# Kernel tuning notes

Hardware: AMD Instinct MI355X
Metric: run time of the kernel (lower is better)

The kernel has to match this reference:

```python
import jax, jax.numpy as jnp
import numpy as np

B, T, N, F = 8, 32, 10000, 16
E = 160000
HG, HT = 64, 128
EPS = 1e-5


def setup_inputs() -> dict:
    key = jax.random.key(0)
    ks = jax.random.split(key, 12)
    s = lambda i, shape, sc=0.05: jax.random.normal(ks[i], shape, dtype=jnp.float32) * sc
    return {
        "x_seq": jax.random.normal(ks[0], (B, T, N, F), dtype=jnp.float32),
        "edge_index": jax.random.randint(ks[1], (2, E), 0, N),
        "W1l": s(2, (HG, F)), "b1": jnp.zeros((HG,), jnp.float32), "W1r": s(3, (HG, F)),
        "g1": jnp.ones((HG,), jnp.float32), "be1": jnp.zeros((HG,), jnp.float32),
        "W2l": s(4, (HG, HG)), "b2": jnp.zeros((HG,), jnp.float32), "W2r": s(5, (HG, HG)),
        "g2": jnp.ones((HG,), jnp.float32), "be2": jnp.zeros((HG,), jnp.float32),
        "W_ih": s(6, (3 * HT, HG)), "W_hh": s(7, (3 * HT, HT)),
        "b_ih": jnp.zeros((3 * HT,), jnp.float32), "b_hh": jnp.zeros((3 * HT,), jnp.float32),
        "Wh": s(8, (1, HT)), "bh": jnp.zeros((1,), jnp.float32),
    }


def _layernorm(h, g, b):
    mu = h.mean(-1, keepdims=True)
    var = ((h - mu) ** 2).mean(-1, keepdims=True)
    return (h - mu) * jax.lax.rsqrt(var + EPS) * g + b


def reference(x_seq, edge_index, W1l, b1, W1r, g1, be1, W2l, b2, W2r, g2, be2,
              W_ih, W_hh, b_ih, b_hh, Wh, bh):
    src, dst = edge_index[0], edge_index[1]
    deg = jax.ops.segment_sum(jnp.ones((E,), x_seq.dtype), dst, num_segments=N)
    inv_deg = (1.0 / jnp.maximum(deg, 1.0))[:, None]  # [N,1]

    def aggregate(x):  # x: [B,N,F] -> mean over incoming neighbors per node
        msgs = x[:, src, :]  # [B,E,F] gather
        agg = jax.vmap(lambda m: jax.ops.segment_sum(m, dst, num_segments=N))(msgs)
        return agg * inv_deg

    def sage(x, Wl, bl, Wr, g, b):
        # PyG SAGEConv(mean): lin_l(agg) + lin_r(x); then LayerNorm + ReLU (dropout=eval)
        h = aggregate(x) @ Wl.T + bl + x @ Wr.T
        return jax.nn.relu(_layernorm(h, g, b))

    def step(_, xt):  # xt: [B,N,F] -> pooled [B,HG]
        h = sage(xt, W1l, b1, W1r, g1, be1)
        h = sage(h, W2l, b2, W2r, g2, be2)
        return None, h.mean(axis=1)

    _, H = jax.lax.scan(step, None, jnp.swapaxes(x_seq, 0, 1))  # [T,B,HG]

    def gru_step(h, x):  # PyTorch GRU gate order: r, z, n
        gi = x @ W_ih.T + b_ih
        gh = h @ W_hh.T + b_hh
        ir, iz, in_ = jnp.split(gi, 3, axis=-1)
        hr, hz, hn = jnp.split(gh, 3, axis=-1)
        r = jax.nn.sigmoid(ir + hr)
        z = jax.nn.sigmoid(iz + hz)
        n = jnp.tanh(in_ + r * hn)
        return (1.0 - z) * n + z * h, None

    h0 = jnp.zeros((x_seq.shape[0], HT), x_seq.dtype)
    ht, _ = jax.lax.scan(gru_step, h0, H)
    return (ht @ Wh.T + bh).squeeze(-1)  # [B]
```

## Files before the change

### kernel.cpp

```cpp
#include <hip/hip_runtime.h>
#include <hip/hip_fp16.h>
#include <math.h>

#define B_ 8
#define T_ 32
#define N_ 10000
#define F_ 16
#define E_ 160000
#define HG_ 64
#define HT_ 128
#define BT_ (B_*T_)
#define PB_ 157
#define EPS_ 1e-5f
#define NR_ (N_+1)

typedef __attribute__((ext_vector_type(8))) _Float16 f16x8_t;
typedef __attribute__((ext_vector_type(4))) float f32x4_t;

__device__ inline unsigned short f2h(float f) {
  return __half_as_ushort(__float2half(f));
}
__device__ inline unsigned pkrtz_u(float a, float b) {
  auto h = __builtin_amdgcn_cvt_pkrtz(a, b);
  unsigned u; __builtin_memcpy(&u, &h, 4); return u;
}
__device__ inline unsigned pack2h(float a, float b) {
  __half2 h = __floats2half2_rn(a, b);
  unsigned u; __builtin_memcpy(&u, &h, 4); return u;
}
__device__ inline __half2 u2h(unsigned u) {
  __half2 h; __builtin_memcpy(&h, &u, 4); return h;
}
__device__ inline unsigned h2u(__half2 h) {
  unsigned u; __builtin_memcpy(&u, &h, 4); return u;
}
__device__ inline void bflyh(__half2& a, int m) {
  unsigned u = (unsigned)__shfl_xor((int)h2u(a), m);
  a += u2h(u);
}

__global__ void k_zero(int* p, int n) {
  int i = blockIdx.x * 256 + threadIdx.x;
  if (i < n) p[i] = 0;
}

__global__ void k_deg(const int* __restrict__ dst, int* __restrict__ deg) {
  int e = blockIdx.x * 256 + threadIdx.x;
  if (e < E_) atomicAdd(&deg[dst[e]], 1);
}

__global__ void k_scan(const int* __restrict__ deg, int* __restrict__ row_ptr,
                       float* __restrict__ inv_deg) {
  __shared__ int part[256];
  int tid = threadIdx.x;
  int base = tid * 40;
  int s = 0;
  for (int i = 0; i < 40; i++) { int idx = base + i; if (idx < N_) s += deg[idx]; }
  part[tid] = s;
  __syncthreads();
  if (tid == 0) {
    int run = 0;
    for (int i = 0; i < 256; i++) { int v = part[i]; part[i] = run; run += v; }
  }
  __syncthreads();
  int run = part[tid];
  for (int i = 0; i < 40; i++) {
    int idx = base + i;
    if (idx < N_) {
      row_ptr[idx] = run;
      int d = deg[idx];
      run += d;
      inv_deg[idx] = 1.0f / fmaxf((float)d, 1.0f);
    } else if (idx == N_) {
      row_ptr[N_] = run;
    }
  }
}

__global__ void k_fill(const int* __restrict__ src, const int* __restrict__ dst,
                       const int* __restrict__ row_ptr, int* __restrict__ cursor,
                       int* __restrict__ col) {
  int e = blockIdx.x * 256 + threadIdx.x;
  if (e < E_) {
    int d = dst[e];
    int p = atomicAdd(&cursor[d], 1);
    col[row_ptr[d] + p] = src[e];
  }
}

__global__ void k_prepw(const float* __restrict__ W2l, const float* __restrict__ W2r,
                        unsigned short* __restrict__ Wbf) {
  int idx = blockIdx.x * 256 + threadIdx.x;
  if (idx >= 4 * 4 * 64 * 8) return;
  int q  = idx & 7;
  int l  = (idx >> 3) & 63;
  int ks = (idx >> 9) & 3;
  int w  = idx >> 11;
  int j = w * 16 + (l & 15);
  int k = ks * 32 + ((l >> 4) * 8) + q;
  float v = (k < 64) ? W2l[j * 64 + k] : W2r[j * 64 + (k - 64)];
  Wbf[idx] = f2h(v);
}

__global__ void k_prepw1(const float* __restrict__ W1l, const float* __restrict__ W1r,
                         unsigned short* __restrict__ Wb1) {
  int idx = blockIdx.x * 256 + threadIdx.x;
  if (idx >= 4 * 64 * 8) return;
  int q = idx & 7;
  int l = (idx >> 3) & 63;
  int w = idx >> 9;
  int j = w * 16 + (l & 15);
  int k = ((l >> 4) * 8) + q;
  float v = (k < 16) ? W1l[j * 16 + k] : W1r[j * 16 + (k - 16)];
  Wb1[idx] = f2h(v);
}

__launch_bounds__(256, 8)
__global__ void k_sage1t(const float* __restrict__ x, const int* __restrict__ row_ptr,
                         const int* __restrict__ col, const float* __restrict__ inv_deg,
                         const unsigned short* __restrict__ Wb1, const float* __restrict__ b1,
                         const float* __restrict__ g1, const float* __restrict__ be1,
                         unsigned short* __restrict__ h1, const float* __restrict__ zrow,
                         int bt0, int CH, int swz) {
  __shared__ __align__(16) unsigned short ZU[64 * 136];
  __shared__ float red[2][4][64];
  unsigned short* Z1b = ZU;
  float* Zf = (float*)ZU;
  int i = blockIdx.x;
  int btl, chunk;
  if (swz) {
    int xcd = i & 7; int j = i >> 3; int per = CH >> 3;
    btl = xcd * per + j / PB_; chunk = j % PB_;
  } else {
    btl = i / PB_; chunk = i % PB_;
  }
  int bt = bt0 + btl;
  size_t xbase = (size_t)bt * (N_ * F_);
  int tid = threadIdx.x;
  int w = __builtin_amdgcn_readfirstlane(tid >> 6);
  int lane = tid & 63;
  int n0 = chunk * 64;
  int node = lane >> 4;
  int eo2 = (lane >> 2) & 3;
  int fq2 = lane & 3;
  const float4* x4b = (const float4*)(x + xbase);
  const float4* z4 = (const float4*)zrow;

  int nloc = n0 + w * 16 + (lane & 15);
  int rpA = 0, dS = 0; float ivS = 0.f;
  if (nloc < N_) { rpA = row_ptr[nloc]; dS = row_ptr[nloc + 1] - rpA; ivS = inv_deg[nloc]; }

  for (int p = 0; p < 4; ++p) {
    int mA = w * 16 + p * 4;
    int nA = n0 + mA;
    int s0My   = __shfl(rpA, p * 4 + node);
    int dMy    = __shfl(dS,  p * 4 + node);
    float ivMy = __shfl(ivS, p * 4 + node);
    int dcMy = dMy > 64 ? 64 : dMy;
    int tmx = max(dcMy, __shfl_xor(dcMy, 16));
    int mx  = max(tmx, __shfl_xor(tmx, 32));
    int rounds = (mx + 3) >> 2;
    int pos = lane & 15;
    int c0r = (pos      < dMy) ? col[s0My + pos]      : 0;
    int c1r = (pos + 16 < dMy) ? col[s0My + pos + 16] : 0;
    int c2r = (pos + 32 < dMy) ? col[s0My + pos + 32] : 0;
    int c3r = (pos + 48 < dMy) ? col[s0My + pos + 48] : 0;
    float4 a = {0.f, 0.f, 0.f, 0.f};
#define S1B(REG, BASE, RR)                                            \
    {                                                                 \
      int idx = eo2 + 4 * (RR);                                       \
      int s = __shfl(REG, (lane & 48) | (idx - (BASE)));              \
      const float4* bp = (idx < dcMy) ? (x4b + (size_t)s * 4) : z4;   \
      float4 v = bp[fq2];                                             \
      a.x += v.x; a.y += v.y; a.z += v.z; a.w += v.w;                 \
    }
    int rounds2 = (rounds + 1) & ~1;
    int r = 0;
    for (; r < rounds2 && r < 4;  r += 2) { S1B(c0r, 0, r)  S1B(c0r, 0, r + 1) }
    for (; r < rounds2 && r < 8;  r += 2) { S1B(c1r, 16, r) S1B(c1r, 16, r + 1) }
    for (; r < rounds2 && r < 12; r += 2) { S1B(c2r, 32, r) S1B(c2r, 32, r + 1) }
    for (; r < rounds2; r += 2)           { S1B(c3r, 48, r) S1B(c3r, 48, r + 1) }
#undef S1B
    if (dMy > 64) {
      for (int e = s0My + 64; e < s0My + dMy; ++e) {
        if (eo2 == 0) {
          float4 v = x4b[(size_t)col[e] * 4 + fq2];
          a.x += v.x; a.y += v.y; a.z += v.z; a.w += v.w;
        }
      }
    }
    a.x += __shfl_xor(a.x, 4);  a.y += __shfl_xor(a.y, 4);
    a.z += __shfl_xor(a.z, 4);  a.w += __shfl_xor(a.w, 4);
    a.x += __shfl_xor(a.x, 8);  a.y += __shfl_xor(a.y, 8);
    a.z += __shfl_xor(a.z, 8);  a.w += __shfl_xor(a.w, 8);
    if (eo2 == 0) {
      uint2 pk;
      pk.x = pkrtz_u(a.x * ivMy, a.y * ivMy);
      pk.y = pkrtz_u(a.z * ivMy, a.w * ivMy);
      *(uint2*)&Z1b[(mA + node) * 40 + fq2 * 4] = pk;
    } else if (eo2 == 1) {
      int nS = nA + node;
      float4 sv = {0.f, 0.f, 0.f, 0.f};
      if (nS < N_) sv = x4b[(size_t)nS * 4 + fq2];
      uint2 pk;
      pk.x = pkrtz_u(sv.x, sv.y);
      pk.y = pkrtz_u(sv.z, sv.w);
      *(uint2*)&Z1b[(mA + node) * 40 + 16 + fq2 * 4] = pk;
    }
  }
  __syncthreads();

  int g = lane >> 4, c = lane & 15;
  float bj = b1[w * 16 + c];
  f32x4_t accf[4];
#pragma unroll
  for (int mt = 0; mt < 4; ++mt) accf[mt] = (f32x4_t){bj, bj, bj, bj};
  f16x8_t bfr = ((const f16x8_t*)Wb1)[w * 64 + lane];
#pragma unroll
  for (int mt = 0; mt < 4; ++mt) {
    const f16x8_t* ap = (const f16x8_t*)&Z1b[(mt * 16 + c) * 40 + g * 8];
    accf[mt] = __builtin_amdgcn_mfma_f32_16x16x32_f16(*ap, bfr, accf[mt], 0, 0, 0);
  }
  __syncthreads();

#pragma unroll
  for (int mt = 0; mt < 4; ++mt) {
#pragma unroll
    for (int q = 0; q < 4; ++q) {
      int nodeq = mt * 16 + g * 4 + q;
      Zf[nodeq * 68 + w * 16 + c] = accf[mt][q];
    }
  }
  __syncthreads();

  int m = lane;
  const float* zr = Zf + m * 68 + w * 16;
  float4 z0 = *(const float4*)(zr + 0);
  float4 z1 = *(const float4*)(zr + 4);
  float4 z2 = *(const float4*)(zr + 8);
  float4 z3 = *(const float4*)(zr + 12);
  float acc[16];
  acc[0] = z0.x; acc[1] = z0.y; acc[2] = z0.z; acc[3] = z0.w;
  acc[4] = z1.x; acc[5] = z1.y; acc[6] = z1.z; acc[7] = z1.w;
  acc[8] = z2.x; acc[9] = z2.y; acc[10] = z2.z; acc[11] = z2.w;
  acc[12] = z3.x; acc[13] = z3.y; acc[14] = z3.z; acc[15] = z3.w;

  float s1 = 0.f, s2 = 0.f;
#pragma unroll
  for (int jj = 0; jj < 16; ++jj) { s1 += acc[jj]; s2 += acc[jj] * acc[jj]; }
  red[0][w][m] = s1;
  red[1][w][m] = s2;
  __syncthreads();
  float mu = (red[0][0][m] + red[0][1][m] + red[0][2][m] + red[0][3][m]) * (1.f / 64.f);
  float ex2 = (red[1][0][m] + red[1][1][m] + red[1][2][m] + red[1][3][m]) * (1.f / 64.f);
  float var = fmaxf(ex2 - mu * mu, 0.f);
  float rs = rsqrtf(var + EPS_);

  int nAbs = n0 + m;
  unsigned short* dst = h1 + ((size_t)btl * NR_ + nAbs) * HG_ + w * 16;
  if (nAbs < N_) {
#pragma unroll
    for (int jj = 0; jj < 16; ++jj)
      acc[jj] = fmaxf((acc[jj] - mu) * rs * g1[w * 16 + jj] + be1[w * 16 + jj], 0.f);
    uint4 pa, pb;
    pa.x = pack2h(acc[0], acc[1]);  pa.y = pack2h(acc[2], acc[3]);
    pa.z = pack2h(acc[4], acc[5]);  pa.w = pack2h(acc[6], acc[7]);
    pb.x = pack2h(acc[8], acc[9]);  pb.y = pack2h(acc[10], acc[11]);
    pb.z = pack2h(acc[12], acc[13]); pb.w = pack2h(acc[14], acc[15]);
    *(uint4*)dst = pa;
    *(uint4*)(dst + 8) = pb;
  } else if (nAbs == N_) {
    uint4 zz = {0, 0, 0, 0};
    *(uint4*)dst = zz;
    *(uint4*)(dst + 8) = zz;
  }
}

__launch_bounds__(256, 8)
__global__ void k_sage2t(const unsigned short* __restrict__ h1, const int* __restrict__ row_ptr,
                         const int* __restrict__ col, const float* __restrict__ inv_deg,
                         const unsigned short* __restrict__ Wbf, const float* __restrict__ b2,
                         const float* __restrict__ g2, const float* __restrict__ be2,
                         float* __restrict__ Hsum, int bt0, int CH, int swz) {
  __shared__ __align__(16) unsigned short Zb[64 * 136];
  __shared__ float red[2][4][64];
  float* Zf = (float*)Zb;
  int i = blockIdx.x;
  int btl, chunk;
  if (swz) {
    int xcd = i & 7; int j = i >> 3; int per = CH >> 3;
    btl = xcd * per + j / PB_; chunk = j % PB_;
  } else {
    btl = i / PB_; chunk = i % PB_;
  }
  int bt = bt0 + btl;
  int b = bt / T_, t = bt % T_;
  const char* h8c = (const char*)(h1 + (size_t)btl * (NR_ * HG_));
  int tid = threadIdx.x;
  int w = __builtin_amdgcn_readfirstlane(tid >> 6);
  int lane = tid & 63;
  int n0 = chunk * 64;
  int nsel = lane >> 5;
  int eo2 = (lane >> 3) & 3;
  int fq3 = lane & 7;
  unsigned foff = (unsigned)fq3 * 16;
  int pos = lane & 31;

  int nloc = n0 + w * 16 + (lane & 15);
  int rpA = 0, dS = 0; float ivS = 0.f;
  if (nloc < N_) { rpA = row_ptr[nloc]; dS = row_ptr[nloc + 1] - rpA; ivS = inv_deg[nloc]; }

  int cp0[8], cp1[8];
#pragma unroll
  for (int p = 0; p < 8; ++p) {
    int s0 = __shfl(rpA, p * 2 + nsel);
    int d  = __shfl(dS,  p * 2 + nsel);
    cp0[p] = (pos      < d) ? col[s0 + pos]      : N_;
    cp1[p] = (pos + 32 < d) ? col[s0 + pos + 32] : N_;
  }

#pragma unroll
  for (int p = 0; p < 8; ++p) {
    int mA = w * 16 + p * 2;
    int s0My   = __shfl(rpA, p * 2 + nsel);
    int dMy    = __shfl(dS,  p * 2 + nsel);
    float ivMy = __shfl(ivS, p * 2 + nsel);
    int dcMy = dMy > 64 ? 64 : dMy;
    int mx = max(dcMy, __shfl_xor(dcMy, 32));
    int rounds = (mx + 3) >> 2;
    __half2 a0 = __float2half2_rn(0.f), a1 = a0, a2 = a0, a3 = a0;
#define S2B(PREG, BASE, RR)                                             \
    {                                                                   \
      int idx = eo2 + 4 * (RR);                                         \
      int s = __shfl(PREG, (lane & 32) | (idx - (BASE)));               \
      uint4 v = *(const uint4*)(h8c + (((unsigned)s << 7) + foff));     \
      a0 += u2h(v.x); a1 += u2h(v.y); a2 += u2h(v.z); a3 += u2h(v.w);   \
    }
    int rounds2 = (rounds + 1) & ~1;
    int r = 0;
    for (; r < rounds2 && r < 8; r += 2) { S2B(cp0[p], 0, r)  S2B(cp0[p], 0, r + 1) }
    for (; r < rounds2; r += 2)          { S2B(cp1[p], 32, r) S2B(cp1[p], 32, r + 1) }
#undef S2B
    if (dMy > 64) {
      for (int e = s0My + 64; e < s0My + dMy; ++e) {
        if (eo2 == 0) {
          uint4 v = *(const uint4*)(h8c + (((unsigned)col[e] << 7) + foff));
          a0 += u2h(v.x); a1 += u2h(v.y); a2 += u2h(v.z); a3 += u2h(v.w);
        }
      }
    }
    bflyh(a0, 8);  bflyh(a1, 8);  bflyh(a2, 8);  bflyh(a3, 8);
    bflyh(a0, 16); bflyh(a1, 16); bflyh(a2, 16); bflyh(a3, 16);
    if (eo2 == 0) {
      __half2 ivh = __float2half2_rn(ivMy);
      uint4 pk;
      pk.x = h2u(a0 * ivh); pk.y = h2u(a1 * ivh);
      pk.z = h2u(a2 * ivh); pk.w = h2u(a3 * ivh);
      *(uint4*)&Zb[(mA + nsel) * 136 + fq3 * 8] = pk;
    } else if (eo2 == 1) {
      int nA = n0 + mA;
      int nS = nA + nsel;
      int nSc = nS < N_ ? nS : N_;
      uint4 sv = *(const uint4*)(h8c + (((unsigned)nSc << 7) + foff));
      *(uint4*)&Zb[(mA + nsel) * 136 + 64 + fq3 * 8] = sv;
    }
  }
  __syncthreads();

  int g = lane >> 4, c = lane & 15;
  const f16x8_t* Wb8 = (const f16x8_t*)Wbf;
  float bj = b2[w * 16 + c];
  f32x4_t accf[4];
#pragma unroll
  for (int mt = 0; mt < 4; ++mt) accf[mt] = (f32x4_t){bj, bj, bj, bj};
#pragma unroll
  for (int ks = 0; ks < 4; ++ks) {
    f16x8_t bfr = Wb8[(w * 4 + ks) * 64 + lane];
#pragma unroll
    for (int mt = 0; mt < 4; ++mt) {
      const f16x8_t* ap = (const f16x8_t*)&Zb[(mt * 16 + c) * 136 + ks * 32 + g * 8];
      accf[mt] = __builtin_amdgcn_mfma_f32_16x16x32_f16(*ap, bfr, accf[mt], 0, 0, 0);
    }
  }
  __syncthreads();

#pragma unroll
  for (int mt = 0; mt < 4; ++mt) {
#pragma unroll
    for (int q = 0; q < 4; ++q) {
      int nodeq = mt * 16 + g * 4 + q;
      Zf[nodeq * 68 + w * 16 + c] = accf[mt][q];
    }
  }
  __syncthreads();

  int m = lane;
  float* zr = Zf + m * 68 + w * 16;
  float4 z0 = *(const float4*)(zr + 0);
  float4 z1 = *(const float4*)(zr + 4);
  float4 z2 = *(const float4*)(zr + 8);
  float4 z3 = *(const float4*)(zr + 12);
  float acc[16];
  acc[0] = z0.x; acc[1] = z0.y; acc[2] = z0.z; acc[3] = z0.w;
  acc[4] = z1.x; acc[5] = z1.y; acc[6] = z1.z; acc[7] = z1.w;
  acc[8] = z2.x; acc[9] = z2.y; acc[10] = z2.z; acc[11] = z2.w;
  acc[12] = z3.x; acc[13] = z3.y; acc[14] = z3.z; acc[15] = z3.w;

  float s1 = 0.f, s2 = 0.f;
#pragma unroll
  for (int jj = 0; jj < 16; ++jj) { s1 += acc[jj]; s2 += acc[jj] * acc[jj]; }
  red[0][w][m] = s1;
  red[1][w][m] = s2;
  __syncthreads();
  float mu = (red[0][0][m] + red[0][1][m] + red[0][2][m] + red[0][3][m]) * (1.f / 64.f);
  float ex2 = (red[1][0][m] + red[1][1][m] + red[1][2][m] + red[1][3][m]) * (1.f / 64.f);
  float var = fmaxf(ex2 - mu * mu, 0.f);
  float rs = rsqrtf(var + EPS_);

  bool okm = (n0 + m) < N_;
#pragma unroll
  for (int jj = 0; jj < 16; ++jj) {
    float hv = fmaxf((acc[jj] - mu) * rs * g2[w * 16 + jj] + be2[w * 16 + jj], 0.f);
    acc[jj] = okm ? hv : 0.f;
  }
  float4 o0 = {acc[0], acc[1], acc[2], acc[3]};
  float4 o1 = {acc[4], acc[5], acc[6], acc[7]};
  float4 o2 = {acc[8], acc[9], acc[10], acc[11]};
  float4 o3 = {acc[12], acc[13], acc[14], acc[15]};
  *(float4*)(zr + 0) = o0;  *(float4*)(zr + 4) = o1;
  *(float4*)(zr + 8) = o2;  *(float4*)(zr + 12) = o3;
  __syncthreads();

  float cs = 0.f;
#pragma unroll
  for (int ii = 0; ii < 16; ++ii) cs += Zf[(w * 16 + ii) * 68 + lane];
  red[0][w][lane] = cs;
  __syncthreads();
  if (w == 0) {
    float tot = red[0][0][lane] + red[0][1][lane] + red[0][2][lane] + red[0][3][lane];
    atomicAdd(&Hsum[(t * B_ + b) * HG_ + lane], tot);
  }
}

__global__ void k_gi(const float* __restrict__ Hsum, const float* __restrict__ W_ih,
                     const float* __restrict__ b_ih, float* __restrict__ GI) {
  __shared__ float xv[64];
  int tb = blockIdx.x;
  int tid = threadIdx.x;
  if (tid < 64) xv[tid] = Hsum[tb * 64 + tid] * (1.0f / (float)N_);
  __syncthreads();
  float g = b_ih[tid];
  const float4* W4 = (const float4*)(W_ih + tid * 64);
  const float4* x4 = (const float4*)xv;
#pragma unroll
  for (int q = 0; q < 16; q++) {
    float4 w = W4[q], xq = x4[q];
    g = fmaf(xq.x, w.x, g); g = fmaf(xq.y, w.y, g);
    g = fmaf(xq.z, w.z, g); g = fmaf(xq.w, w.w, g);
  }
  GI[tb * 384 + tid] = g;
}

__global__ void k_gru(const float* __restrict__ GI, const float* __restrict__ W_hh,
                      const float* __restrict__ b_hh, const float* __restrict__ Wh,
                      const float* __restrict__ bh, float* __restrict__ out) {
  __shared__ float hL[128];
  __shared__ float ghL[384];
  __shared__ float red[128];
  int b = blockIdx.x, tid = threadIdx.x;
  if (tid < 128) hL[tid] = 0.f;
  float bhh = b_hh[tid];
  const float4* W4 = (const float4*)(W_hh + tid * 128);
  for (int t = 0; t < T_; ++t) {
    __syncthreads();
    float g = bhh;
    const float4* h4 = (const float4*)hL;
#pragma unroll
    for (int q = 0; q < 32; q++) {
      float4 w = W4[q], hv = h4[q];
      g = fmaf(hv.x, w.x, g); g = fmaf(hv.y, w.y, g);
      g = fmaf(hv.z, w.z, g); g = fmaf(hv.w, w.w, g);
    }
    ghL[tid] = g;
    __syncthreads();
    float hnew = 0.f;
    if (tid < 128) {
      const float* gi = GI + (t * B_ + b) * 384;
      float rr = 1.f / (1.f + expf(-(gi[tid] + ghL[tid])));
      float zz = 1.f / (1.f + expf(-(gi[128 + tid] + ghL[128 + tid])));
      float nn = tanhf(gi[256 + tid] + rr * ghL[256 + tid]);
      hnew = (1.f - zz) * nn + zz * hL[tid];
    }
    __syncthreads();
    if (tid < 128) hL[tid] = hnew;
  }
  __syncthreads();
  if (tid < 128) red[tid] = hL[tid] * Wh[tid];
  __syncthreads();
  if (tid == 0) {
    float s = bh[0];
    for (int k = 0; k < 128; k++) s += red[k];
    out[b] = s;
  }
}

extern "C" void kernel_launch(void* const* d_in, const int* in_sizes, int n_in,
                              void* d_out, int out_size, void* d_ws, size_t ws_size,
                              hipStream_t stream) {
  const float* x    = (const float*)d_in[0];
  const int*   ei   = (const int*)d_in[1];
  const float* W1l  = (const float*)d_in[2];
  const float* b1   = (const float*)d_in[3];
  const float* W1r  = (const float*)d_in[4];
  const float* g1   = (const float*)d_in[5];
  const float* be1  = (const float*)d_in[6];
  const float* W2l  = (const float*)d_in[7];
  const float* b2   = (const float*)d_in[8];
  const float* W2r  = (const float*)d_in[9];
  const float* g2   = (const float*)d_in[10];
  const float* be2  = (const float*)d_in[11];
  const float* W_ih = (const float*)d_in[12];
  const float* W_hh = (const float*)d_in[13];
  const float* b_ih = (const float*)d_in[14];
  const float* b_hh = (const float*)d_in[15];
  const float* Wh   = (const float*)d_in[16];
  const float* bh   = (const float*)d_in[17];
  float* out = (float*)d_out;

  char* ws = (char*)d_ws;
  size_t off = 0;
  auto alloc = [&](size_t bytes) { void* p = ws + off; off += (bytes + 255) & ~(size_t)255; return p; };
  int*   deg     = (int*)alloc((size_t)N_ * 4);
  int*   row_ptr = (int*)alloc((size_t)(N_ + 1) * 4);
  int*   cursor  = (int*)alloc((size_t)N_ * 4);
  int*   col     = (int*)alloc((size_t)E_ * 4);
  float* ivd     = (float*)alloc((size_t)N_ * 4);
  float* Hsum    = (float*)alloc((size_t)BT_ * HG_ * 4);
  float* GI      = (float*)alloc((size_t)BT_ * 384 * 4);
  unsigned short* Wbf = (unsigned short*)alloc((size_t)4 * 4 * 64 * 8 * 2);
  unsigned short* Wb1 = (unsigned short*)alloc((size_t)4 * 64 * 8 * 2);
  float* zrowp   = (float*)alloc(256);
  size_t fixed = off;
  unsigned short* h1 = (unsigned short*)(ws + off);

  size_t cap = (ws_size > fixed) ? (ws_size - fixed) : 0;
  int CH = (int)(cap / ((size_t)NR_ * HG_ * 2));
  if (CH > 64) CH = 64;
  if (CH >= 8) CH &= ~7;
  if (CH < 1) CH = 1;

  int zn = (int)(fixed / 4);
  k_zero<<<(zn + 255) / 256, 256, 0, stream>>>((int*)ws, zn);

  const int* srcp = ei;
  const int* dstp = ei + E_;
  k_deg<<<(E_ + 255) / 256, 256, 0, stream>>>(dstp, deg);
  k_scan<<<1, 256, 0, stream>>>(deg, row_ptr, ivd);
  k_fill<<<(E_ + 255) / 256, 256, 0, stream>>>(srcp, dstp, row_ptr, cursor, col);
  k_prepw<<<32, 256, 0, stream>>>(W2l, W2r, Wbf);
  k_prepw1<<<8, 256, 0, stream>>>(W1l, W1r, Wb1);

  for (int bt0 = 0; bt0 < BT_; bt0 += CH) {
    int c = BT_ - bt0 < CH ? BT_ - bt0 : CH;
    int swz = (c % 8 == 0) ? 1 : 0;
    k_sage1t<<<c * PB_, 256, 0, stream>>>(x, row_ptr, col, ivd, Wb1, b1, g1, be1,
                                          h1, zrowp, bt0, c, swz);
    k_sage2t<<<c * PB_, 256, 0, stream>>>(h1, row_ptr, col, ivd, Wbf, b2, g2, be2,
                                          Hsum, bt0, c, swz);
  }
  k_gi<<<BT_, 384, 0, stream>>>(Hsum, W_ih, b_ih, GI);
  k_gru<<<B_, 384, 0, stream>>>(GI, W_hh, b_hh, Wh, bh, out);
}
```

Before: 1.164 ms.

## Software-pipeline SAGE layers by fusing layer1 of chunk k with layer2 of chunk k-1

Merges the two SAGE layer kernels into one launch whose blocks pick a role: layer 1 for the current chunk of (batch,time) slices, or layer 2 for the previous chunk. The h1 intermediate is double-buffered, so the two stages work on different buffers and overlap inside one grid. Role assignment can be interleaved across XCD groups. This removes the serialization and tail idle between the separate layer launches and halves the launch count. The cost is a larger workspace, which caps the chunk size at 32 instead of 64, and register pressure from a kernel body holding both roles.

```diff
diff --git a/kernel.cpp b/kernel.cpp
--- a/kernel.cpp
+++ b/kernel.cpp
@@ -115,21 +115,19 @@
   Wb1[idx] = f2h(v);
 }
 
-__launch_bounds__(256, 8)
-__global__ void k_sage1t(const float* __restrict__ x, const int* __restrict__ row_ptr,
-                         const int* __restrict__ col, const float* __restrict__ inv_deg,
-                         const unsigned short* __restrict__ Wb1, const float* __restrict__ b1,
-                         const float* __restrict__ g1, const float* __restrict__ be1,
-                         unsigned short* __restrict__ h1, const float* __restrict__ zrow,
-                         int bt0, int CH, int swz) {
-  __shared__ __align__(16) unsigned short ZU[64 * 136];
-  __shared__ float red[2][4][64];
+__device__ __forceinline__ void sage1_body(
+    int i, unsigned short* ZU, float (*red)[4][64],
+    const float* __restrict__ x, const int* __restrict__ row_ptr,
+    const int* __restrict__ col, const float* __restrict__ inv_deg,
+    const unsigned short* __restrict__ Wb1, const float* __restrict__ b1,
+    const float* __restrict__ g1, const float* __restrict__ be1,
+    unsigned short* __restrict__ h1, const float* __restrict__ zrow,
+    int bt0, int CHc, int swz) {
   unsigned short* Z1b = ZU;
   float* Zf = (float*)ZU;
-  int i = blockIdx.x;
   int btl, chunk;
   if (swz) {
-    int xcd = i & 7; int j = i >> 3; int per = CH >> 3;
+    int xcd = i & 7; int j = i >> 3; int per = CHc >> 3;
     btl = xcd * per + j / PB_; chunk = j % PB_;
   } else {
     btl = i / PB_; chunk = i % PB_;
@@ -276,19 +274,18 @@
   }
 }
 
-__launch_bounds__(256, 8)
-__global__ void k_sage2t(const unsigned short* __restrict__ h1, const int* __restrict__ row_ptr,
-                         const int* __restrict__ col, const float* __restrict__ inv_deg,
-                         const unsigned short* __restrict__ Wbf, const float* __restrict__ b2,
-                         const float* __restrict__ g2, const float* __restrict__ be2,
-                         float* __restrict__ Hsum, int bt0, int CH, int swz) {
-  __shared__ __align__(16) unsigned short Zb[64 * 136];
-  __shared__ float red[2][4][64];
-  float* Zf = (float*)Zb;
-  int i = blockIdx.x;
+__device__ __forceinline__ void sage2_body(
+    int i, unsigned short* ZU, float (*red)[4][64],
+    const unsigned short* __restrict__ h1, const int* __restrict__ row_ptr,
+    const int* __restrict__ col, const float* __restrict__ inv_deg,
+    const unsigned short* __restrict__ Wbf, const float* __restrict__ b2,
+    const float* __restrict__ g2, const float* __restrict__ be2,
+    float* __restrict__ Hsum, int bt0, int CHc, int swz) {
+  unsigned short* Zb = ZU;
+  float* Zf = (float*)ZU;
   int btl, chunk;
   if (swz) {
-    int xcd = i & 7; int j = i >> 3; int per = CH >> 3;
+    int xcd = i & 7; int j = i >> 3; int per = CHc >> 3;
     btl = xcd * per + j / PB_; chunk = j % PB_;
   } else {
     btl = i / PB_; chunk = i % PB_;
@@ -440,6 +437,32 @@
     float tot = red[0][0][lane] + red[0][1][lane] + red[0][2][lane] + red[0][3][lane];
     atomicAdd(&Hsum[(t * B_ + b) * HG_ + lane], tot);
   }
+}
+
+__launch_bounds__(256, 8)
+__global__ void k_pipe(const float* __restrict__ x, const int* __restrict__ row_ptr,
+                       const int* __restrict__ col, const float* __restrict__ ivd,
+                       const unsigned short* __restrict__ Wb1, const float* __restrict__ b1,
+                       const float* __restrict__ g1, const float* __restrict__ be1,
+                       const unsigned short* __restrict__ Wbf, const float* __restrict__ b2,
+                       const float* __restrict__ g2, const float* __restrict__ be2,
+                       const unsigned short* __restrict__ h1in, unsigned short* __restrict__ h1out,
+                       float* __restrict__ Hsum, const float* __restrict__ zrow,
+                       int bt0_1, int c1, int swz1, int bt0_2, int c2, int swz2, int ilv) {
+  __shared__ __align__(16) unsigned short ZU[64 * 136];
+  __shared__ float red[2][4][64];
+  int i = blockIdx.x;
+  int role, li;
+  if (c1 == 0)      { role = 1; li = i; }
+  else if (c2 == 0) { role = 0; li = i; }
+  else if (ilv)     { int g = i >> 3; role = g & 1; li = ((g >> 1) << 3) | (i & 7); }
+  else              { int off = c1 * PB_; role = (i >= off) ? 1 : 0; li = role ? i - off : i; }
+  if (role == 0)
+    sage1_body(li, ZU, red, x, row_ptr, col, ivd, Wb1, b1, g1, be1, h1out, zrow,
+               bt0_1, c1, swz1);
+  else
+    sage2_body(li, ZU, red, h1in, row_ptr, col, ivd, Wbf, b2, g2, be2, Hsum,
+               bt0_2, c2, swz2);
 }
 
 __global__ void k_gi(const float* __restrict__ Hsum, const float* __restrict__ W_ih,
@@ -541,13 +564,16 @@
   unsigned short* Wb1 = (unsigned short*)alloc((size_t)4 * 64 * 8 * 2);
   float* zrowp   = (float*)alloc(256);
   size_t fixed = off;
-  unsigned short* h1 = (unsigned short*)(ws + off);
-
+
+  size_t rowb = (size_t)NR_ * HG_ * 2;
   size_t cap = (ws_size > fixed) ? (ws_size - fixed) : 0;
-  int CH = (int)(cap / ((size_t)NR_ * HG_ * 2));
-  if (CH > 64) CH = 64;
-  if (CH >= 8) CH &= ~7;
-  if (CH < 1) CH = 1;
+  int CHP = (int)(cap / (2 * rowb));
+  int CH;
+  if (CHP >= 32) CH = 32;
+  else if (CHP >= 8) CH = CHP & ~7;
+  else CH = CHP < 1 ? 1 : CHP;
+  unsigned short* h1a = (unsigned short*)(ws + fixed);
+  unsigned short* h1b = (unsigned short*)((char*)h1a + (size_t)CH * rowb);
 
   int zn = (int)(fixed / 4);
   k_zero<<<(zn + 255) / 256, 256, 0, stream>>>((int*)ws, zn);
@@ -560,13 +586,22 @@
   k_prepw<<<32, 256, 0, stream>>>(W2l, W2r, Wbf);
   k_prepw1<<<8, 256, 0, stream>>>(W1l, W1r, Wb1);
 
-  for (int bt0 = 0; bt0 < BT_; bt0 += CH) {
-    int c = BT_ - bt0 < CH ? BT_ - bt0 : CH;
-    int swz = (c % 8 == 0) ? 1 : 0;
-    k_sage1t<<<c * PB_, 256, 0, stream>>>(x, row_ptr, col, ivd, Wb1, b1, g1, be1,
-                                          h1, zrowp, bt0, c, swz);
-    k_sage2t<<<c * PB_, 256, 0, stream>>>(h1, row_ptr, col, ivd, Wbf, b2, g2, be2,
-                                          Hsum, bt0, c, swz);
+  int nch = (BT_ + CH - 1) / CH;
+  for (int k = 0; k <= nch; ++k) {
+    int b0_1 = k * CH;
+    int c1 = (k < nch) ? (BT_ - b0_1 < CH ? BT_ - b0_1 : CH) : 0;
+    int b0_2 = (k - 1) * CH;
+    int c2 = (k > 0) ? (BT_ - b0_2 < CH ? BT_ - b0_2 : CH) : 0;
+    unsigned short* h1out = (k & 1) ? h1b : h1a;
+    const unsigned short* h1in = (k & 1) ? h1a : h1b;
+    int swz1 = (c1 > 0 && (c1 % 8) == 0) ? 1 : 0;
+    int swz2 = (c2 > 0 && (c2 % 8) == 0) ? 1 : 0;
+    int ilv = (c1 == c2 && ((c1 * PB_) & 7) == 0) ? 1 : 0;
+    int grid = (c1 + c2) * PB_;
+    if (grid > 0)
+      k_pipe<<<grid, 256, 0, stream>>>(x, row_ptr, col, ivd, Wb1, b1, g1, be1,
+                                       Wbf, b2, g2, be2, h1in, h1out, Hsum, zrowp,
+                                       b0_1, c1, swz1, b0_2, c2, swz2, ilv);
   }
   k_gi<<<BT_, 384, 0, stream>>>(Hsum, W_ih, b_ih, GI);
   k_gru<<<B_, 384, 0, stream>>>(GI, W_hh, b_hh, Wh, bh, out);
```

Result: slower. 1.231 ms (+5.8%).

## Split aggregation from transforms and interleave 8 timesteps per node row

Applied to the files above, without the earlier changes.

Each SAGE layer is split into a gather-aggregation kernel and a dense MFMA transform kernel. Before gathering, inputs are repacked into a layout where each node row holds the features of 8 batch-time slots contiguously, so one neighbor index fetch serves 8 slices and each gather reads a wider contiguous row. This is meant to amortize CSR index loads and improve gather coalescing. In exchange it adds an extra transpose pass and intermediate buffers (xg, agg1, agg2) round-tripped through global memory, plus more kernel launches.

```diff
diff --git a/kernel.cpp b/kernel.cpp
--- a/kernel.cpp
+++ b/kernel.cpp
@@ -12,7 +12,8 @@
 #define BT_ (B_*T_)
 #define PB_ 157
 #define EPS_ 1e-5f
-#define NR_ (N_+1)
+#define NR2_ (PB_*64)
+#define NBTG_ 32
 
 typedef __attribute__((ext_vector_type(8))) _Float16 f16x8_t;
 typedef __attribute__((ext_vector_type(4))) float f32x4_t;
@@ -33,10 +34,6 @@
 }
 __device__ inline unsigned h2u(__half2 h) {
   unsigned u; __builtin_memcpy(&u, &h, 4); return u;
-}
-__device__ inline void bflyh(__half2& a, int m) {
-  unsigned u = (unsigned)__shfl_xor((int)h2u(a), m);
-  a += u2h(u);
 }
 
 __global__ void k_zero(int* p, int n) {
@@ -115,98 +112,138 @@
   Wb1[idx] = f2h(v);
 }
 
+__global__ void k_xg(const float* __restrict__ x, float* __restrict__ xg,
+                     int g0) {
+  int i = blockIdx.x;
+  int btgl = i / PB_, chunk = i % PB_;
+  int t = threadIdx.x;
+  int node = t >> 2, fq = t & 3;
+  int ng = chunk * 64 + node;
+  int nc = ng < N_ ? ng : N_ - 1;
+  float* ob = xg + ((size_t)btgl * NR2_ + ng) * 128 + fq * 4;
+#pragma unroll
+  for (int slot = 0; slot < 8; ++slot) {
+    int bt = (g0 + btgl) * 8 + slot;
+    float4 v = *(const float4*)(x + ((size_t)bt * N_ + nc) * 16 + fq * 4);
+    *(float4*)(ob + slot * 16) = v;
+  }
+}
+
 __launch_bounds__(256, 8)
-__global__ void k_sage1t(const float* __restrict__ x, const int* __restrict__ row_ptr,
-                         const int* __restrict__ col, const float* __restrict__ inv_deg,
-                         const unsigned short* __restrict__ Wb1, const float* __restrict__ b1,
-                         const float* __restrict__ g1, const float* __restrict__ be1,
-                         unsigned short* __restrict__ h1, const float* __restrict__ zrow,
-                         int bt0, int CH, int swz) {
+__global__ void k_agg1(const float* __restrict__ xg, const int* __restrict__ row_ptr,
+                       const int* __restrict__ col, const float* __restrict__ inv_deg,
+                       float* __restrict__ agg1) {
+  int i = blockIdx.x;
+  int btgl = i / PB_, chunk = i % PB_;
+  int tid = threadIdx.x;
+  int w = __builtin_amdgcn_readfirstlane(tid >> 6);
+  int lane = tid & 63;
+  int eo = lane >> 5, slot = (lane >> 2) & 7, fq = lane & 3;
+  const float* xb = xg + (size_t)btgl * NR2_ * 128;
+  float* ab = agg1 + (size_t)btgl * NR2_ * 128;
+  int nbase = chunk * 64 + w * 16;
+  unsigned off = (unsigned)slot * 16 + (unsigned)fq * 4;
+  for (int nn = 0; nn < 16; ++nn) {
+    int dn = nbase + nn;
+    float4 acc = {0.f, 0.f, 0.f, 0.f};
+    int dd = 0, s0 = 0; float iv = 0.f;
+    if (dn < N_) { s0 = row_ptr[dn]; dd = row_ptr[dn + 1] - s0; iv = inv_deg[dn]; }
+    for (int base = 0; base < dd; base += 64) {
+      int cnt = dd - base; if (cnt > 64) cnt = 64;
+      int cl = (lane < cnt) ? col[s0 + base + lane] : 0;
+      for (int e = 0; e < cnt; e += 2) {
+        int idx = e + eo;
+        int s = __shfl(cl, idx);
+        if (idx < cnt) {
+          float4 v = *(const float4*)(xb + (size_t)s * 128 + off);
+          acc.x += v.x; acc.y += v.y; acc.z += v.z; acc.w += v.w;
+        }
+      }
+    }
+    acc.x += __shfl_xor(acc.x, 32); acc.y += __shfl_xor(acc.y, 32);
+    acc.z += __shfl_xor(acc.z, 32); acc.w += __shfl_xor(acc.w, 32);
+    if (eo == 0) {
+      acc.x *= iv; acc.y *= iv; acc.z *= iv; acc.w *= iv;
+      *(float4*)(ab + (size_t)dn * 128 + off) = acc;
+    }
+  }
+}
+
+__launch_bounds__(256, 8)
+__global__ void k_agg2(const unsigned short* __restrict__ h1g, const int* __restrict__ row_ptr,
+                       const int* __restrict__ col, const float* __restrict__ inv_deg,
+                       unsigned short* __restrict__ agg2) {
+  int i = blockIdx.x;
+  int btgl = i / PB_, chunk = i % PB_;
+  int tid = threadIdx.x;
+  int w = __builtin_amdgcn_readfirstlane(tid >> 6);
+  int lane = tid & 63;
+  int slot = lane >> 3, fq3 = lane & 7;
+  const char* hb = (const char*)(h1g + (size_t)btgl * NR2_ * 512);
+  char* ab = (char*)(agg2 + (size_t)btgl * NR2_ * 512);
+  int nbase = chunk * 64 + w * 16;
+  unsigned off = (unsigned)slot * 128 + (unsigned)fq3 * 16;
+  for (int nn = 0; nn < 16; ++nn) {
+    int dn = nbase + nn;
+    __half2 a0 = __float2half2_rn(0.f), a1 = a0, a2 = a0, a3 = a0;
+    int dd = 0, s0 = 0; float iv = 0.f;
+    if (dn < N_) { s0 = row_ptr[dn]; dd = row_ptr[dn + 1] - s0; iv = inv_deg[dn]; }
+    for (int base = 0; base < dd; base += 64) {
+      int cnt = dd - base; if (cnt > 64) cnt = 64;
+      int cl = (lane < cnt) ? col[s0 + base + lane] : 0;
+      int e = 0;
+      for (; e + 1 < cnt; e += 2) {
+        int sA = __shfl(cl, e), sB = __shfl(cl, e + 1);
+        uint4 vA = *(const uint4*)(hb + (((size_t)sA) << 10) + off);
+        uint4 vB = *(const uint4*)(hb + (((size_t)sB) << 10) + off);
+        a0 += u2h(vA.x); a1 += u2h(vA.y); a2 += u2h(vA.z); a3 += u2h(vA.w);
+        a0 += u2h(vB.x); a1 += u2h(vB.y); a2 += u2h(vB.z); a3 += u2h(vB.w);
+      }
+      if (e < cnt) {
+        int sA = __shfl(cl, e);
+        uint4 vA = *(const uint4*)(hb + (((size_t)sA) << 10) + off);
+        a0 += u2h(vA.x); a1 += u2h(vA.y); a2 += u2h(vA.z); a3 += u2h(vA.w);
+      }
+    }
+    __half2 ivh = __float2half2_rn(iv);
+    uint4 pk;
+    pk.x = h2u(a0 * ivh); pk.y = h2u(a1 * ivh);
+    pk.z = h2u(a2 * ivh); pk.w = h2u(a3 * ivh);
+    *(uint4*)(ab + (((size_t)dn) << 10) + off) = pk;
+  }
+}
+
+__launch_bounds__(256, 8)
+__global__ void k_tr1(const float* __restrict__ x, const float* __restrict__ agg1,
+                      const unsigned short* __restrict__ Wb1, const float* __restrict__ b1,
+                      const float* __restrict__ g1, const float* __restrict__ be1,
+                      unsigned short* __restrict__ h1g, int g0) {
   __shared__ __align__(16) unsigned short ZU[64 * 136];
   __shared__ float red[2][4][64];
   unsigned short* Z1b = ZU;
   float* Zf = (float*)ZU;
   int i = blockIdx.x;
-  int btl, chunk;
-  if (swz) {
-    int xcd = i & 7; int j = i >> 3; int per = CH >> 3;
-    btl = xcd * per + j / PB_; chunk = j % PB_;
-  } else {
-    btl = i / PB_; chunk = i % PB_;
-  }
-  int bt = bt0 + btl;
-  size_t xbase = (size_t)bt * (N_ * F_);
+  int btl = i / PB_, chunk = i % PB_;
+  int bt = g0 * 8 + btl;
+  int btgl = btl >> 3, slot = btl & 7;
   int tid = threadIdx.x;
   int w = __builtin_amdgcn_readfirstlane(tid >> 6);
   int lane = tid & 63;
   int n0 = chunk * 64;
-  int node = lane >> 4;
-  int eo2 = (lane >> 2) & 3;
-  int fq2 = lane & 3;
-  const float4* x4b = (const float4*)(x + xbase);
-  const float4* z4 = (const float4*)zrow;
-
-  int nloc = n0 + w * 16 + (lane & 15);
-  int rpA = 0, dS = 0; float ivS = 0.f;
-  if (nloc < N_) { rpA = row_ptr[nloc]; dS = row_ptr[nloc + 1] - rpA; ivS = inv_deg[nloc]; }
-
-  for (int p = 0; p < 4; ++p) {
-    int mA = w * 16 + p * 4;
-    int nA = n0 + mA;
-    int s0My   = __shfl(rpA, p * 4 + node);
-    int dMy    = __shfl(dS,  p * 4 + node);
-    float ivMy = __shfl(ivS, p * 4 + node);
-    int dcMy = dMy > 64 ? 64 : dMy;
-    int tmx = max(dcMy, __shfl_xor(dcMy, 16));
-    int mx  = max(tmx, __shfl_xor(tmx, 32));
-    int rounds = (mx + 3) >> 2;
-    int pos = lane & 15;
-    int c0r = (pos      < dMy) ? col[s0My + pos]      : 0;
-    int c1r = (pos + 16 < dMy) ? col[s0My + pos + 16] : 0;
-    int c2r = (pos + 32 < dMy) ? col[s0My + pos + 32] : 0;
-    int c3r = (pos + 48 < dMy) ? col[s0My + pos + 48] : 0;
-    float4 a = {0.f, 0.f, 0.f, 0.f};
-#define S1B(REG, BASE, RR)                                            \
-    {                                                                 \
-      int idx = eo2 + 4 * (RR);                                       \
-      int s = __shfl(REG, (lane & 48) | (idx - (BASE)));              \
-      const float4* bp = (idx < dcMy) ? (x4b + (size_t)s * 4) : z4;   \
-      float4 v = bp[fq2];                                             \
-      a.x += v.x; a.y += v.y; a.z += v.z; a.w += v.w;                 \
-    }
-    int rounds2 = (rounds + 1) & ~1;
-    int r = 0;
-    for (; r < rounds2 && r < 4;  r += 2) { S1B(c0r, 0, r)  S1B(c0r, 0, r + 1) }
-    for (; r < rounds2 && r < 8;  r += 2) { S1B(c1r, 16, r) S1B(c1r, 16, r + 1) }
-    for (; r < rounds2 && r < 12; r += 2) { S1B(c2r, 32, r) S1B(c2r, 32, r + 1) }
-    for (; r < rounds2; r += 2)           { S1B(c3r, 48, r) S1B(c3r, 48, r + 1) }
-#undef S1B
-    if (dMy > 64) {
-      for (int e = s0My + 64; e < s0My + dMy; ++e) {
-        if (eo2 == 0) {
-          float4 v = x4b[(size_t)col[e] * 4 + fq2];
-          a.x += v.x; a.y += v.y; a.z += v.z; a.w += v.w;
-        }
-      }
-    }
-    a.x += __shfl_xor(a.x, 4);  a.y += __shfl_xor(a.y, 4);
-    a.z += __shfl_xor(a.z, 4);  a.w += __shfl_xor(a.w, 4);
-    a.x += __shfl_xor(a.x, 8);  a.y += __shfl_xor(a.y, 8);
-    a.z += __shfl_xor(a.z, 8);  a.w += __shfl_xor(a.w, 8);
-    if (eo2 == 0) {
-      uint2 pk;
-      pk.x = pkrtz_u(a.x * ivMy, a.y * ivMy);
-      pk.y = pkrtz_u(a.z * ivMy, a.w * ivMy);
-      *(uint2*)&Z1b[(mA + node) * 40 + fq2 * 4] = pk;
-    } else if (eo2 == 1) {
-      int nS = nA + node;
-      float4 sv = {0.f, 0.f, 0.f, 0.f};
-      if (nS < N_) sv = x4b[(size_t)nS * 4 + fq2];
-      uint2 pk;
-      pk.x = pkrtz_u(sv.x, sv.y);
-      pk.y = pkrtz_u(sv.z, sv.w);
-      *(uint2*)&Z1b[(mA + node) * 40 + 16 + fq2 * 4] = pk;
-    }
+
+  {
+    int m = w * 16 + (lane >> 2), fq2 = lane & 3;
+    int ng = n0 + m;
+    const float* ab = agg1 + (size_t)btgl * NR2_ * 128;
+    float4 av = *(const float4*)(ab + (size_t)ng * 128 + slot * 16 + fq2 * 4);
+    float4 sv = {0.f, 0.f, 0.f, 0.f};
+    if (ng < N_) sv = *(const float4*)(x + ((size_t)bt * N_ + ng) * 16 + fq2 * 4);
+    uint2 pka;
+    pka.x = pkrtz_u(av.x, av.y);  pka.y = pkrtz_u(av.z, av.w);
+    *(uint2*)&Z1b[m * 40 + fq2 * 4] = pka;
+    uint2 pks;
+    pks.x = pkrtz_u(sv.x, sv.y);  pks.y = pkrtz_u(sv.z, sv.w);
+    *(uint2*)&Z1b[m * 40 + 16 + fq2 * 4] = pks;
   }
   __syncthreads();
 
@@ -257,7 +294,7 @@
   float rs = rsqrtf(var + EPS_);
 
   int nAbs = n0 + m;
-  unsigned short* dst = h1 + ((size_t)btl * NR_ + nAbs) * HG_ + w * 16;
+  unsigned short* dst = h1g + ((size_t)btgl * NR2_ + nAbs) * 512 + slot * 64 + w * 16;
   if (nAbs < N_) {
 #pragma unroll
     for (int jj = 0; jj < 16; ++jj)
@@ -269,7 +306,7 @@
     pb.z = pack2h(acc[12], acc[13]); pb.w = pack2h(acc[14], acc[15]);
     *(uint4*)dst = pa;
     *(uint4*)(dst + 8) = pb;
-  } else if (nAbs == N_) {
+  } else {
     uint4 zz = {0, 0, 0, 0};
     *(uint4*)dst = zz;
     *(uint4*)(dst + 8) = zz;
@@ -277,92 +314,36 @@
 }
 
 __launch_bounds__(256, 8)
-__global__ void k_sage2t(const unsigned short* __restrict__ h1, const int* __restrict__ row_ptr,
-                         const int* __restrict__ col, const float* __restrict__ inv_deg,
-                         const unsigned short* __restrict__ Wbf, const float* __restrict__ b2,
-                         const float* __restrict__ g2, const float* __restrict__ be2,
-                         float* __restrict__ Hsum, int bt0, int CH, int swz) {
+__global__ void k_tr2(const unsigned short* __restrict__ h1g, const unsigned short* __restrict__ agg2,
+                      const unsigned short* __restrict__ Wbf, const float* __restrict__ b2,
+                      const float* __restrict__ g2, const float* __restrict__ be2,
+                      float* __restrict__ Hsum, int g0) {
   __shared__ __align__(16) unsigned short Zb[64 * 136];
   __shared__ float red[2][4][64];
   float* Zf = (float*)Zb;
   int i = blockIdx.x;
-  int btl, chunk;
-  if (swz) {
-    int xcd = i & 7; int j = i >> 3; int per = CH >> 3;
-    btl = xcd * per + j / PB_; chunk = j % PB_;
-  } else {
-    btl = i / PB_; chunk = i % PB_;
-  }
-  int bt = bt0 + btl;
+  int btl = i / PB_, chunk = i % PB_;
+  int bt = g0 * 8 + btl;
+  int btgl = btl >> 3, slot = btl & 7;
   int b = bt / T_, t = bt % T_;
-  const char* h8c = (const char*)(h1 + (size_t)btl * (NR_ * HG_));
   int tid = threadIdx.x;
   int w = __builtin_amdgcn_readfirstlane(tid >> 6);
   int lane = tid & 63;
   int n0 = chunk * 64;
-  int nsel = lane >> 5;
-  int eo2 = (lane >> 3) & 3;
-  int fq3 = lane & 7;
-  unsigned foff = (unsigned)fq3 * 16;
-  int pos = lane & 31;
-
-  int nloc = n0 + w * 16 + (lane & 15);
-  int rpA = 0, dS = 0; float ivS = 0.f;
-  if (nloc < N_) { rpA = row_ptr[nloc]; dS = row_ptr[nloc + 1] - rpA; ivS = inv_deg[nloc]; }
-
-  int cp0[8], cp1[8];
-#pragma unroll
-  for (int p = 0; p < 8; ++p) {
-    int s0 = __shfl(rpA, p * 2 + nsel);
-    int d  = __shfl(dS,  p * 2 + nsel);
-    cp0[p] = (pos      < d) ? col[s0 + pos]      : N_;
-    cp1[p] = (pos + 32 < d) ? col[s0 + pos + 32] : N_;
-  }
-
-#pragma unroll
-  for (int p = 0; p < 8; ++p) {
-    int mA = w * 16 + p * 2;
-    int s0My   = __shfl(rpA, p * 2 + nsel);
-    int dMy    = __shfl(dS,  p * 2 + nsel);
-    float ivMy = __shfl(ivS, p * 2 + nsel);
-    int dcMy = dMy > 64 ? 64 : dMy;
-    int mx = max(dcMy, __shfl_xor(dcMy, 32));
-    int rounds = (mx + 3) >> 2;
-    __half2 a0 = __float2half2_rn(0.f), a1 = a0, a2 = a0, a3 = a0;
-#define S2B(PREG, BASE, RR)                                             \
-    {                                                                   \
-      int idx = eo2 + 4 * (RR);                                         \
-      int s = __shfl(PREG, (lane & 32) | (idx - (BASE)));               \
-      uint4 v = *(const uint4*)(h8c + (((unsigned)s << 7) + foff));     \
-      a0 += u2h(v.x); a1 += u2h(v.y); a2 += u2h(v.z); a3 += u2h(v.w);   \
-    }
-    int rounds2 = (rounds + 1) & ~1;
-    int r = 0;
-    for (; r < rounds2 && r < 8; r += 2) { S2B(cp0[p], 0, r)  S2B(cp0[p], 0, r + 1) }
-    for (; r < rounds2; r += 2)          { S2B(cp1[p], 32, r) S2B(cp1[p], 32, r + 1) }
-#undef S2B
-    if (dMy > 64) {
-      for (int e = s0My + 64; e < s0My + dMy; ++e) {
-        if (eo2 == 0) {
-          uint4 v = *(const uint4*)(h8c + (((unsigned)col[e] << 7) + foff));
-          a0 += u2h(v.x); a1 += u2h(v.y); a2 += u2h(v.z); a3 += u2h(v.w);
-        }
-      }
-    }
-    bflyh(a0, 8);  bflyh(a1, 8);  bflyh(a2, 8);  bflyh(a3, 8);
-    bflyh(a0, 16); bflyh(a1, 16); bflyh(a2, 16); bflyh(a3, 16);
-    if (eo2 == 0) {
-      __half2 ivh = __float2half2_rn(ivMy);
-      uint4 pk;
-      pk.x = h2u(a0 * ivh); pk.y = h2u(a1 * ivh);
-      pk.z = h2u(a2 * ivh); pk.w = h2u(a3 * ivh);
-      *(uint4*)&Zb[(mA + nsel) * 136 + fq3 * 8] = pk;
-    } else if (eo2 == 1) {
-      int nA = n0 + mA;
-      int nS = nA + nsel;
-      int nSc = nS < N_ ? nS : N_;
-      uint4 sv = *(const uint4*)(h8c + (((unsigned)nSc << 7) + foff));
-      *(uint4*)&Zb[(mA + nsel) * 136 + 64 + fq3 * 8] = sv;
+
+  {
+    int mh = lane >> 3, fq3 = lane & 7;
+    const char* ab = (const char*)(agg2 + (size_t)btgl * NR2_ * 512);
+    const char* hb = (const char*)(h1g + (size_t)btgl * NR2_ * 512);
+    unsigned off = (unsigned)slot * 128 + (unsigned)fq3 * 16;
+#pragma unroll
+    for (int p = 0; p < 2; ++p) {
+      int m = w * 16 + p * 8 + mh;
+      size_t ro = (((size_t)(n0 + m)) << 10) + off;
+      uint4 va = *(const uint4*)(ab + ro);
+      uint4 vs = *(const uint4*)(hb + ro);
+      *(uint4*)&Zb[m * 136 + fq3 * 8] = va;
+      *(uint4*)&Zb[m * 136 + 64 + fq3 * 8] = vs;
     }
   }
   __syncthreads();
@@ -539,15 +520,21 @@
   float* GI      = (float*)alloc((size_t)BT_ * 384 * 4);
   unsigned short* Wbf = (unsigned short*)alloc((size_t)4 * 4 * 64 * 8 * 2);
   unsigned short* Wb1 = (unsigned short*)alloc((size_t)4 * 64 * 8 * 2);
-  float* zrowp   = (float*)alloc(256);
   size_t fixed = off;
-  unsigned short* h1 = (unsigned short*)(ws + off);
-
+
+  size_t xg_b = (size_t)NR2_ * 128 * 4;
+  size_t a1_b = xg_b;
+  size_t h1_b = (size_t)NR2_ * 512 * 2;
+  size_t a2_b = h1_b;
+  size_t per = xg_b + a1_b + h1_b + a2_b;
   size_t cap = (ws_size > fixed) ? (ws_size - fixed) : 0;
-  int CH = (int)(cap / ((size_t)NR_ * HG_ * 2));
-  if (CH > 64) CH = 64;
-  if (CH >= 8) CH &= ~7;
-  if (CH < 1) CH = 1;
+  int SG = (int)(cap / per);
+  if (SG > NBTG_) SG = NBTG_;
+  if (SG < 1) SG = 1;
+  float* xg = (float*)(ws + fixed);
+  float* agg1 = (float*)((char*)xg + (size_t)SG * xg_b);
+  unsigned short* h1g = (unsigned short*)((char*)agg1 + (size_t)SG * a1_b);
+  unsigned short* agg2 = (unsigned short*)((char*)h1g + (size_t)SG * h1_b);
 
   int zn = (int)(fixed / 4);
   k_zero<<<(zn + 255) / 256, 256, 0, stream>>>((int*)ws, zn);
@@ -560,13 +547,13 @@
   k_prepw<<<32, 256, 0, stream>>>(W2l, W2r, Wbf);
   k_prepw1<<<8, 256, 0, stream>>>(W1l, W1r, Wb1);
 
-  for (int bt0 = 0; bt0 < BT_; bt0 += CH) {
-    int c = BT_ - bt0 < CH ? BT_ - bt0 : CH;
-    int swz = (c % 8 == 0) ? 1 : 0;
-    k_sage1t<<<c * PB_, 256, 0, stream>>>(x, row_ptr, col, ivd, Wb1, b1, g1, be1,
-                                          h1, zrowp, bt0, c, swz);
-    k_sage2t<<<c * PB_, 256, 0, stream>>>(h1, row_ptr, col, ivd, Wbf, b2, g2, be2,
-                                          Hsum, bt0, c, swz);
+  for (int g0 = 0; g0 < NBTG_; g0 += SG) {
+    int nb = NBTG_ - g0 < SG ? NBTG_ - g0 : SG;
+    k_xg  <<<nb * PB_, 256, 0, stream>>>(x, xg, g0);
+    k_agg1<<<nb * PB_, 256, 0, stream>>>(xg, row_ptr, col, ivd, agg1);
+    k_tr1 <<<nb * 8 * PB_, 256, 0, stream>>>(x, agg1, Wb1, b1, g1, be1, h1g, g0);
+    k_agg2<<<nb * PB_, 256, 0, stream>>>(h1g, row_ptr, col, ivd, agg2);
+    k_tr2 <<<nb * 8 * PB_, 256, 0, stream>>>(h1g, agg2, Wbf, b2, g2, be2, Hsum, g0);
   }
   k_gi<<<BT_, 384, 0, stream>>>(Hsum, W_ih, b_ih, GI);
   k_gru<<<B_, 384, 0, stream>>>(GI, W_hh, b_hh, Wh, bh, out);
```

New measurement: 1.846 ms. +58.5%, slower.
